# Optimization experiments

Hardware: AMD Instinct MI355X
Metric: run time of the kernel (lower is better)

## Reference

```python
import jax, jax.numpy as jnp
import numpy as np

B, T, HID = 4, 2048, 2048
NH = 16
HD = HID // NH  # 128
THETA = 10000.0


def _rope_cache(seq_len, head_dim):
    half = head_dim // 2
    freqs = 1.0 / THETA ** (jnp.arange(half, dtype=jnp.float32) / half)
    pos = jnp.arange(seq_len, dtype=jnp.float32)
    angles = pos[:, None] * freqs[None, :]  # [T, hd/2]
    return jnp.cos(angles), jnp.sin(angles)


def _apply_rope(x, cos, sin):
    # x: [B, nh, T, hd]; cos/sin: [T, hd/2]
    x_even, x_odd = x[..., 0::2], x[..., 1::2]
    c = cos[None, None, :, :]
    s = sin[None, None, :, :]
    rot_even = x_even * c - x_odd * s
    rot_odd = x_even * s + x_odd * c
    # interleave back: stack on new last axis then flatten
    return jnp.stack([rot_even, rot_odd], axis=-1).reshape(x.shape)


def setup_inputs() -> dict:
    key = jax.random.key(0)
    k1, k2, k3, k4 = jax.random.split(key, 4)
    x = jax.random.normal(k1, (B, T, HID), dtype=jnp.float32)
    w_qkv = jax.random.normal(k2, (3 * HID, HID), dtype=jnp.float32) * 0.02
    w_proj = jax.random.normal(k3, (HID, HID), dtype=jnp.float32) * 0.02
    b_proj = jax.random.normal(k4, (HID,), dtype=jnp.float32) * 0.02
    cos, sin = _rope_cache(T, HD)
    return {"x": x, "w_qkv": w_qkv, "w_proj": w_proj, "b_proj": b_proj,
            "cos": cos, "sin": sin}


def reference(x, w_qkv, w_proj, b_proj, cos, sin):
    Bx, Tx, Hx = x.shape
    qkv = jnp.einsum('bth,oh->bto', x, w_qkv)  # [B,T,3H]
    qkv = qkv.reshape(Bx, Tx, 3, NH, HD)
    q = jnp.transpose(qkv[:, :, 0], (0, 2, 1, 3))  # [B,nh,T,hd]
    k = jnp.transpose(qkv[:, :, 1], (0, 2, 1, 3))
    v = jnp.transpose(qkv[:, :, 2], (0, 2, 1, 3))
    q = _apply_rope(q, cos, sin)
    k = _apply_rope(k, cos, sin)
    scale = 1.0 / np.sqrt(HD).astype(np.float32)
    scores = jnp.einsum('bhqd,bhkd->bhqk', q, k) * scale  # [B,nh,T,T]
    attn = jax.nn.softmax(scores, axis=-1)
    out = jnp.einsum('bhqk,bhkd->bhqd', attn, v)  # [B,nh,T,hd]
    out = jnp.transpose(out, (0, 2, 1, 3)).reshape(Bx, Tx, Hx)
    return jnp.einsum('bth,oh->bto', out, w_proj) + b_proj
```

## Files before the change

### kernel.cpp

```cpp
#include <hip/hip_runtime.h>
#include <stdint.h>


typedef unsigned short u16;
typedef unsigned int   u32;
typedef unsigned long long u64;
typedef __attribute__((ext_vector_type(8))) short short8;
typedef __attribute__((ext_vector_type(4))) float f32x4;

__device__ __forceinline__ void gload16(const void* g, void* l) {
  __builtin_amdgcn_global_load_lds((const __attribute__((address_space(1))) void*)g,
                                   (__attribute__((address_space(3))) void*)l, 16, 0, 0);
}

__device__ __forceinline__ u16 f2bf(float f) {
  u32 u = __builtin_bit_cast(u32, f);
  u32 r = (u + 0x7fffu + ((u >> 16) & 1u)) >> 16;
  return (u16)r;
}
__device__ __forceinline__ float bf2f(u16 b) {
  u32 u = ((u32)b) << 16;
  return __builtin_bit_cast(float, u);
}

__global__ __launch_bounds__(256) void cvt_kernel(const float* __restrict__ src,
                                                  u16* __restrict__ dst) {
  size_t i = ((size_t)blockIdx.x * 256 + threadIdx.x) * 4;
  f32x4 v = *(const f32x4*)(src + i);
  u64 pk = (u64)f2bf(v[0]) | ((u64)f2bf(v[1]) << 16) |
           ((u64)f2bf(v[2]) << 32) | ((u64)f2bf(v[3]) << 48);
  *(u64*)(dst + i) = pk;
}

template <int MODE>
__global__ __launch_bounds__(256, 2) void gemm_bt(const u16* __restrict__ A,
                                                  const u16* __restrict__ B,
                                                  void* __restrict__ C,
                                                  int M, int N, int K,
                                                  const float* __restrict__ bias) {
  __shared__ __attribute__((aligned(16))) u16 As[128 * 32];
  __shared__ __attribute__((aligned(16))) u16 Bs[128 * 32];
  const int tid  = threadIdx.x;
  const int wave = tid >> 6, lane = tid & 63;
  const int quad = lane >> 4, l16 = lane & 15;
  const int m0 = blockIdx.y * 128, n0 = blockIdx.x * 128;
  const int wr = wave >> 1, wc = wave & 1;
  const int lrow = lane >> 2;
  const int lcol = (lane & 3) * 8;
  f32x4 acc[4][4] = {};

  const size_t Abase = (size_t)(m0 + wave * 32 + lrow) * K + lcol;
  const size_t Bbase = (size_t)(n0 + wave * 32 + lrow) * K + lcol;

  for (int k0 = 0; k0 < K; k0 += 32) {
    gload16(A + Abase + k0,                 &As[(wave * 32) * 32]);
    gload16(A + Abase + (size_t)16 * K + k0, &As[(wave * 32 + 16) * 32]);
    gload16(B + Bbase + k0,                 &Bs[(wave * 32) * 32]);
    gload16(B + Bbase + (size_t)16 * K + k0, &Bs[(wave * 32 + 16) * 32]);
    __syncthreads();
    short8 a[4], b[4];
#pragma unroll
    for (int rt = 0; rt < 4; rt++)
      a[rt] = *(const short8*)&As[(wr * 64 + rt * 16 + l16) * 32 + quad * 8];
#pragma unroll
    for (int ct = 0; ct < 4; ct++)
      b[ct] = *(const short8*)&Bs[(wc * 64 + ct * 16 + l16) * 32 + quad * 8];
#pragma unroll
    for (int rt = 0; rt < 4; rt++)
#pragma unroll
      for (int ct = 0; ct < 4; ct++)
        acc[rt][ct] = __builtin_amdgcn_mfma_f32_16x16x32_bf16(a[rt], b[ct], acc[rt][ct], 0, 0, 0);
    __syncthreads();
  }
#pragma unroll
  for (int rt = 0; rt < 4; rt++) {
#pragma unroll
    for (int ct = 0; ct < 4; ct++) {
      const int col = n0 + wc * 64 + ct * 16 + l16;
      float bv = (MODE == 1) ? bias[col] : 0.0f;
#pragma unroll
      for (int r = 0; r < 4; r++) {
        const int row = m0 + wr * 64 + rt * 16 + quad * 4 + r;
        if (MODE == 0)
          ((u16*)C)[(size_t)row * N + col] = f2bf(acc[rt][ct][r]);
        else
          ((float*)C)[(size_t)row * N + col] = acc[rt][ct][r] + bv;
      }
    }
  }
}

__global__ __launch_bounds__(256) void rope_reshape(const u16* __restrict__ qkv,
                                                    const float* __restrict__ cosb,
                                                    const float* __restrict__ sinb,
                                                    u16* __restrict__ Qr,
                                                    u16* __restrict__ Kr,
                                                    u16* __restrict__ Vt) {
  __shared__ __attribute__((aligned(16))) u16 Vl[32 * 132];
  const int tb = blockIdx.x;
  const int bh = blockIdx.y;
  const int tid = threadIdx.x;
  const int b = bh >> 4, h = bh & 15;
  const float scale = 0.08838834764831845f;
#pragma unroll
  for (int p8 = 0; p8 < 8; p8++) {
    int p = p8 * 256 + tid;
    int r = p >> 6, i = p & 63;
    int t = tb * 32 + r;
    size_t base = (size_t)(b * 2048 + t) * 6144 + h * 128 + 2 * i;
    float c = cosb[t * 64 + i], s = sinb[t * 64 + i];
    u32 q2 = *(const u32*)(qkv + base);
    float qe = bf2f((u16)q2), qo = bf2f((u16)(q2 >> 16));
    u32 qw = (u32)f2bf((qe * c - qo * s) * scale) | ((u32)f2bf((qe * s + qo * c) * scale) << 16);
    *(u32*)(Qr + ((size_t)bh * 2048 + t) * 128 + 2 * i) = qw;
    u32 k2 = *(const u32*)(qkv + base + 2048);
    float ke = bf2f((u16)k2), ko = bf2f((u16)(k2 >> 16));
    u32 kw = (u32)f2bf(ke * c - ko * s) | ((u32)f2bf(ke * s + ko * c) << 16);
    *(u32*)(Kr + ((size_t)bh * 2048 + t) * 128 + 2 * i) = kw;
    u32 v2 = *(const u32*)(qkv + base + 4096);
    *(u32*)&Vl[r * 132 + 2 * i] = v2;
  }
  __syncthreads();
#pragma unroll
  for (int u8 = 0; u8 < 8; u8++) {
    int u = u8 * 256 + tid;
    int d = u >> 4, tp = (u & 15) * 2;
    u32 lo = Vl[tp * 132 + d];
    u32 hi = Vl[(tp + 1) * 132 + d];
    *(u32*)(Vt + ((size_t)bh * 128 + d) * 2048 + tb * 32 + tp) = lo | (hi << 16);
  }
}

__global__ __launch_bounds__(256, 2) void flash_attn(const u16* __restrict__ Q,
                                                     const u16* __restrict__ K,
                                                     const u16* __restrict__ Vt,
                                                     u16* __restrict__ Out) {
  __shared__ __attribute__((aligned(16))) char lds[67584];
  u16* Klds = (u16*)lds;
  u16* Vlds = (u16*)(lds + 34816);
  const int qb = blockIdx.x;
  const int bh = blockIdx.y;
  const int tid = threadIdx.x;
  const int wave = tid >> 6, lane = tid & 63;
  const int quad = lane >> 4, l16 = lane & 15;
  const int lrow4 = lane >> 2, lcol8 = (lane & 3) * 8;
  const u16* Qh = Q + (size_t)bh * 2048 * 128;
  const u16* Kh = K + (size_t)bh * 2048 * 128;
  const u16* Vh = Vt + (size_t)bh * 128 * 2048;

  short8 qf[2][4];
#pragma unroll
  for (int rt = 0; rt < 2; rt++)
#pragma unroll
    for (int kk = 0; kk < 4; kk++)
      qf[rt][kk] = *(const short8*)(Qh + (size_t)(qb * 128 + wave * 32 + rt * 16 + l16) * 128 + kk * 32 + quad * 8);

  f32x4 o[2][8] = {};
  float mrow[2][4], lrowv[2][4];
#pragma unroll
  for (int rt = 0; rt < 2; rt++)
#pragma unroll
    for (int r = 0; r < 4; r++) { mrow[rt][r] = -1e30f; lrowv[rt][r] = 0.f; }

  for (int kb = 0; kb < 16; kb++) {
    __syncthreads();
#pragma unroll
    for (int c = 0; c < 8; c++) {
      int ch = wave * 8 + c;
      int tbb = ch >> 2, kk = ch & 3;
      gload16(Kh + (size_t)(kb * 128 + tbb * 16 + lrow4) * 128 + kk * 32 + lcol8, &Klds[ch * 512]);
      gload16(Vh + (size_t)(tbb * 16 + lrow4) * 2048 + kb * 128 + kk * 32 + lcol8, &Vlds[ch * 512]);
    }
    __syncthreads();

    f32x4 s[2][8];
#pragma unroll
    for (int nt = 0; nt < 8; nt++) {
      short8 kf[4];
#pragma unroll
      for (int kk = 0; kk < 4; kk++)
        kf[kk] = *(const short8*)&Klds[(nt * 4 + kk) * 512 + l16 * 32 + quad * 8];
#pragma unroll
      for (int rt = 0; rt < 2; rt++) {
        f32x4 a = {};
#pragma unroll
        for (int kk = 0; kk < 4; kk++)
          a = __builtin_amdgcn_mfma_f32_16x16x32_bf16(qf[rt][kk], kf[kk], a, 0, 0, 0);
        s[rt][nt] = a;
      }
    }

#pragma unroll
    for (int rt = 0; rt < 2; rt++)
#pragma unroll
      for (int r = 0; r < 4; r++) {
        float mx8 = s[rt][0][r];
#pragma unroll
        for (int nt = 1; nt < 8; nt++) mx8 = fmaxf(mx8, s[rt][nt][r]);
        if (__any(mx8 > mrow[rt][r] + 8.0f)) {
          float mx = mx8;
          mx = fmaxf(mx, __shfl_xor(mx, 1));
          mx = fmaxf(mx, __shfl_xor(mx, 2));
          mx = fmaxf(mx, __shfl_xor(mx, 4));
          mx = fmaxf(mx, __shfl_xor(mx, 8));
          float mnew = fmaxf(mrow[rt][r], mx);
          float alpha = __expf(mrow[rt][r] - mnew);
          mrow[rt][r] = mnew;
          lrowv[rt][r] *= alpha;
#pragma unroll
          for (int dt = 0; dt < 8; dt++) o[rt][dt][r] *= alpha;
        }
        float m = mrow[rt][r];
        float sum = 0.f;
#pragma unroll
        for (int nt = 0; nt < 8; nt++) {
          float p = __expf(s[rt][nt][r] - m);
          s[rt][nt][r] = p;
          sum += p;
        }
        sum += __shfl_xor(sum, 1);
        sum += __shfl_xor(sum, 2);
        sum += __shfl_xor(sum, 4);
        sum += __shfl_xor(sum, 8);
        lrowv[rt][r] += sum;
      }

    __syncthreads();
    u16* P = (u16*)lds + wave * 4352;
#pragma unroll
    for (int rt = 0; rt < 2; rt++)
#pragma unroll
      for (int nt = 0; nt < 8; nt++)
#pragma unroll
        for (int r = 0; r < 4; r++)
          P[(rt * 16 + quad * 4 + r) * 136 + nt * 16 + l16] = f2bf(s[rt][nt][r]);
    __syncthreads();

#pragma unroll
    for (int kk = 0; kk < 4; kk++) {
      short8 pf[2];
#pragma unroll
      for (int rt = 0; rt < 2; rt++)
        pf[rt] = *(const short8*)&P[(rt * 16 + l16) * 136 + kk * 32 + quad * 8];
#pragma unroll
      for (int dt = 0; dt < 8; dt++) {
        short8 vf = *(const short8*)&Vlds[(dt * 4 + kk) * 512 + l16 * 32 + quad * 8];
#pragma unroll
        for (int rt = 0; rt < 2; rt++)
          o[rt][dt] = __builtin_amdgcn_mfma_f32_16x16x32_bf16(pf[rt], vf, o[rt][dt], 0, 0, 0);
      }
    }
  }

  const int b = bh >> 4, h = bh & 15;
#pragma unroll
  for (int rt = 0; rt < 2; rt++) {
    float inv[4];
#pragma unroll
    for (int r = 0; r < 4; r++) inv[r] = 1.0f / lrowv[rt][r];
#pragma unroll
    for (int dt = 0; dt < 8; dt++) {
      int d = dt * 16 + l16;
#pragma unroll
      for (int r = 0; r < 4; r++) {
        int t = qb * 128 + wave * 32 + rt * 16 + quad * 4 + r;
        Out[((size_t)(b * 2048 + t)) * 2048 + h * 128 + d] = f2bf(o[rt][dt][r] * inv[r]);
      }
    }
  }
}

extern "C" void kernel_launch(void* const* d_in, const int* in_sizes, int n_in,
                              void* d_out, int out_size, void* d_ws, size_t ws_size,
                              hipStream_t stream) {
  const float* x      = (const float*)d_in[0];
  const float* w_qkv  = (const float*)d_in[1];
  const float* w_proj = (const float*)d_in[2];
  const float* b_proj = (const float*)d_in[3];
  const float* cosb   = (const float*)d_in[4];
  const float* sinb   = (const float*)d_in[5];
  char* ws = (char*)d_ws;
  const size_t MB = 1024 * 1024;
  u16* xb   = (u16*)(ws + 0);
  u16* Qr   = (u16*)(ws + 0);
  u16* wqb  = (u16*)(ws + 32 * MB);
  u16* Kr   = (u16*)(ws + 32 * MB);
  u16* qkv  = (u16*)(ws + 64 * MB);
  u16* attn = (u16*)(ws + 64 * MB);
  u16* Vt   = (u16*)(ws + 160 * MB);
  u16* wpb  = (u16*)(ws + 192 * MB);

  cvt_kernel<<<16384, 256, 0, stream>>>(x, xb);
  cvt_kernel<<<12288, 256, 0, stream>>>(w_qkv, wqb);
  cvt_kernel<<<4096, 256, 0, stream>>>(w_proj, wpb);

  gemm_bt<0><<<dim3(48, 64), 256, 0, stream>>>(xb, wqb, qkv, 8192, 6144, 2048, nullptr);
  rope_reshape<<<dim3(64, 64), 256, 0, stream>>>(qkv, cosb, sinb, Qr, Kr, Vt);
  flash_attn<<<dim3(16, 64), 256, 0, stream>>>(Qr, Kr, Vt, attn);
  gemm_bt<1><<<dim3(16, 64), 256, 0, stream>>>(attn, wpb, (float*)d_out, 8192, 2048, 2048, b_proj);
}
```

Measured before the change: 702.9 us.

## Fuse RoPE and head reshape into QKV GEMM epilogue

Replaces the separate rope_reshape kernel by applying rotary embedding, the query scale, and the head-major/transposed-V layout directly in the QKV GEMM epilogue, using a lane shuffle to pair even/odd elements. This removes the intermediate qkv buffer write and re-read plus one kernel launch. In exchange, the epilogue does strided 2-byte and transposed 8-byte global stores and per-element cos/sin loads, which may coalesce poorly. Workspace offsets are reorganized because the buffers no longer alias.

Measured after the change: 692.1 us. About the same (-1.5%).

```diff
diff --git a/kernel.cpp b/kernel.cpp
--- a/kernel.cpp
+++ b/kernel.cpp
@@ -32,10 +32,92 @@
   *(u64*)(dst + i) = pk;
 }
 
-template <int MODE>
+__global__ __launch_bounds__(256, 2) void gemm_qkv_rope(const u16* __restrict__ A,
+                                                        const u16* __restrict__ B,
+                                                        const float* __restrict__ cosb,
+                                                        const float* __restrict__ sinb,
+                                                        u16* __restrict__ Qr,
+                                                        u16* __restrict__ Kr,
+                                                        u16* __restrict__ Vt) {
+  const int K = 2048;
+  __shared__ __attribute__((aligned(16))) u16 As[128 * 32];
+  __shared__ __attribute__((aligned(16))) u16 Bs[128 * 32];
+  const int tid  = threadIdx.x;
+  const int wave = tid >> 6, lane = tid & 63;
+  const int quad = lane >> 4, l16 = lane & 15;
+  const int m0 = blockIdx.y * 128, n0 = blockIdx.x * 128;
+  const int wr = wave >> 1, wc = wave & 1;
+  const int lrow = lane >> 2;
+  const int lcol = (lane & 3) * 8;
+  f32x4 acc[4][4] = {};
+
+  const size_t Abase = (size_t)(m0 + wave * 32 + lrow) * K + lcol;
+  const size_t Bbase = (size_t)(n0 + wave * 32 + lrow) * K + lcol;
+
+  for (int k0 = 0; k0 < K; k0 += 32) {
+    gload16(A + Abase + k0,                 &As[(wave * 32) * 32]);
+    gload16(A + Abase + (size_t)16 * K + k0, &As[(wave * 32 + 16) * 32]);
+    gload16(B + Bbase + k0,                 &Bs[(wave * 32) * 32]);
+    gload16(B + Bbase + (size_t)16 * K + k0, &Bs[(wave * 32 + 16) * 32]);
+    __syncthreads();
+    short8 a[4], b[4];
+#pragma unroll
+    for (int rt = 0; rt < 4; rt++)
+      a[rt] = *(const short8*)&As[(wr * 64 + rt * 16 + l16) * 32 + quad * 8];
+#pragma unroll
+    for (int ct = 0; ct < 4; ct++)
+      b[ct] = *(const short8*)&Bs[(wc * 64 + ct * 16 + l16) * 32 + quad * 8];
+#pragma unroll
+    for (int rt = 0; rt < 4; rt++)
+#pragma unroll
+      for (int ct = 0; ct < 4; ct++)
+        acc[rt][ct] = __builtin_amdgcn_mfma_f32_16x16x32_bf16(a[rt], b[ct], acc[rt][ct], 0, 0, 0);
+    __syncthreads();
+  }
+
+  const int which = n0 >> 11;
+  const int h = (n0 >> 7) & 15;
+  if (which == 2) {
+#pragma unroll
+    for (int rt = 0; rt < 4; rt++) {
+#pragma unroll
+      for (int ct = 0; ct < 4; ct++) {
+        const int d = wc * 64 + ct * 16 + l16;
+        const int row0 = m0 + wr * 64 + rt * 16 + quad * 4;
+        const int b = row0 >> 11, tt0 = row0 & 2047;
+        u64 pk = (u64)f2bf(acc[rt][ct][0]) | ((u64)f2bf(acc[rt][ct][1]) << 16) |
+                 ((u64)f2bf(acc[rt][ct][2]) << 32) | ((u64)f2bf(acc[rt][ct][3]) << 48);
+        *(u64*)(Vt + ((size_t)((b * 16 + h) * 128 + d)) * 2048 + tt0) = pk;
+      }
+    }
+  } else {
+    u16* dst = which ? Kr : Qr;
+    const float qs = which ? 1.0f : 0.08838834764831845f;
+#pragma unroll
+    for (int rt = 0; rt < 4; rt++) {
+#pragma unroll
+      for (int ct = 0; ct < 4; ct++) {
+        const int d = wc * 64 + ct * 16 + l16;
+        const float sgn = (d & 1) ? 1.0f : -1.0f;
+        const int ci = d >> 1;
+#pragma unroll
+        for (int r = 0; r < 4; r++) {
+          const int row = m0 + wr * 64 + rt * 16 + quad * 4 + r;
+          const int b = row >> 11, tt = row & 2047;
+          const float c = cosb[tt * 64 + ci], s = sinb[tt * 64 + ci];
+          const float v = acc[rt][ct][r];
+          const float p = __shfl_xor(v, 1);
+          const float rot = (v * c + sgn * p * s) * qs;
+          dst[((size_t)((b * 16 + h) * 2048 + tt)) * 128 + d] = f2bf(rot);
+        }
+      }
+    }
+  }
+}
+
 __global__ __launch_bounds__(256, 2) void gemm_bt(const u16* __restrict__ A,
                                                   const u16* __restrict__ B,
-                                                  void* __restrict__ C,
+                                                  float* __restrict__ C,
                                                   int M, int N, int K,
                                                   const float* __restrict__ bias) {
   __shared__ __attribute__((aligned(16))) u16 As[128 * 32];
@@ -77,57 +159,13 @@
 #pragma unroll
     for (int ct = 0; ct < 4; ct++) {
       const int col = n0 + wc * 64 + ct * 16 + l16;
-      float bv = (MODE == 1) ? bias[col] : 0.0f;
+      float bv = bias[col];
 #pragma unroll
       for (int r = 0; r < 4; r++) {
         const int row = m0 + wr * 64 + rt * 16 + quad * 4 + r;
-        if (MODE == 0)
-          ((u16*)C)[(size_t)row * N + col] = f2bf(acc[rt][ct][r]);
-        else
-          ((float*)C)[(size_t)row * N + col] = acc[rt][ct][r] + bv;
-      }
-    }
-  }
-}
-
-__global__ __launch_bounds__(256) void rope_reshape(const u16* __restrict__ qkv,
-                                                    const float* __restrict__ cosb,
-                                                    const float* __restrict__ sinb,
-                                                    u16* __restrict__ Qr,
-                                                    u16* __restrict__ Kr,
-                                                    u16* __restrict__ Vt) {
-  __shared__ __attribute__((aligned(16))) u16 Vl[32 * 132];
-  const int tb = blockIdx.x;
-  const int bh = blockIdx.y;
-  const int tid = threadIdx.x;
-  const int b = bh >> 4, h = bh & 15;
-  const float scale = 0.08838834764831845f;
-#pragma unroll
-  for (int p8 = 0; p8 < 8; p8++) {
-    int p = p8 * 256 + tid;
-    int r = p >> 6, i = p & 63;
-    int t = tb * 32 + r;
-    size_t base = (size_t)(b * 2048 + t) * 6144 + h * 128 + 2 * i;
-    float c = cosb[t * 64 + i], s = sinb[t * 64 + i];
-    u32 q2 = *(const u32*)(qkv + base);
-    float qe = bf2f((u16)q2), qo = bf2f((u16)(q2 >> 16));
-    u32 qw = (u32)f2bf((qe * c - qo * s) * scale) | ((u32)f2bf((qe * s + qo * c) * scale) << 16);
-    *(u32*)(Qr + ((size_t)bh * 2048 + t) * 128 + 2 * i) = qw;
-    u32 k2 = *(const u32*)(qkv + base + 2048);
-    float ke = bf2f((u16)k2), ko = bf2f((u16)(k2 >> 16));
-    u32 kw = (u32)f2bf(ke * c - ko * s) | ((u32)f2bf(ke * s + ko * c) << 16);
-    *(u32*)(Kr + ((size_t)bh * 2048 + t) * 128 + 2 * i) = kw;
-    u32 v2 = *(const u32*)(qkv + base + 4096);
-    *(u32*)&Vl[r * 132 + 2 * i] = v2;
-  }
-  __syncthreads();
-#pragma unroll
-  for (int u8 = 0; u8 < 8; u8++) {
-    int u = u8 * 256 + tid;
-    int d = u >> 4, tp = (u & 15) * 2;
-    u32 lo = Vl[tp * 132 + d];
-    u32 hi = Vl[(tp + 1) * 132 + d];
-    *(u32*)(Vt + ((size_t)bh * 128 + d) * 2048 + tb * 32 + tp) = lo | (hi << 16);
+        C[(size_t)row * N + col] = acc[rt][ct][r] + bv;
+      }
+    }
   }
 }
 
@@ -282,20 +320,18 @@
   char* ws = (char*)d_ws;
   const size_t MB = 1024 * 1024;
   u16* xb   = (u16*)(ws + 0);
-  u16* Qr   = (u16*)(ws + 0);
   u16* wqb  = (u16*)(ws + 32 * MB);
-  u16* Kr   = (u16*)(ws + 32 * MB);
-  u16* qkv  = (u16*)(ws + 64 * MB);
-  u16* attn = (u16*)(ws + 64 * MB);
-  u16* Vt   = (u16*)(ws + 160 * MB);
-  u16* wpb  = (u16*)(ws + 192 * MB);
+  u16* wpb  = (u16*)(ws + 56 * MB);
+  u16* Qr   = (u16*)(ws + 64 * MB);
+  u16* Kr   = (u16*)(ws + 96 * MB);
+  u16* Vt   = (u16*)(ws + 128 * MB);
+  u16* attn = (u16*)(ws + 160 * MB);
 
   cvt_kernel<<<16384, 256, 0, stream>>>(x, xb);
   cvt_kernel<<<12288, 256, 0, stream>>>(w_qkv, wqb);
   cvt_kernel<<<4096, 256, 0, stream>>>(w_proj, wpb);
 
-  gemm_bt<0><<<dim3(48, 64), 256, 0, stream>>>(xb, wqb, qkv, 8192, 6144, 2048, nullptr);
-  rope_reshape<<<dim3(64, 64), 256, 0, stream>>>(qkv, cosb, sinb, Qr, Kr, Vt);
+  gemm_qkv_rope<<<dim3(48, 64), 256, 0, stream>>>(xb, wqb, cosb, sinb, Qr, Kr, Vt);
   flash_attn<<<dim3(16, 64), 256, 0, stream>>>(Qr, Kr, Vt, attn);
-  gemm_bt<1><<<dim3(16, 64), 256, 0, stream>>>(attn, wpb, (float*)d_out, 8192, 2048, 2048, b_proj);
-}
+  gemm_bt<<<dim3(16, 64), 256, 0, stream>>>(attn, wpb, (float*)d_out, 8192, 2048, 2048, b_proj);
+}
```
